# Performance work log

Hardware: AMD Instinct MI355X
Metric: run time of the kernel (lower is better)

The kernel has to match this reference:

```python
import jax, jax.numpy as jnp
from jax import lax
import numpy as np

RF = 1024   # receptive field
MGC = 60    # mgc feature size
UPS = 200   # upsample factor
MIX = 10    # num mixtures
FS = 256    # filter size
F = 2       # mgc frames
N = F * UPS
SQRT_HALF = 0.70710678118


def setup_inputs() -> dict:
    key = jax.random.key(0)
    ks = jax.random.split(key, 30)
    g = lambda i, shape, s=0.05: jax.random.normal(ks[i], shape, dtype=jnp.float32) * s
    return dict(
        signal=g(0, (N + RF,), 0.3),
        mgc=g(1, (F, MGC), 1.0),
        cond_w=g(2, (MGC * UPS, MGC)), cond_b=g(3, (MGC * UPS,)),
        l0_win=g(4, (FS, 1, 2)), l0_bin=g(5, (FS,)),
        l0_wg=g(6, (FS, 1, 2)), l0_bg=g(7, (FS,)),
        l0_wr=g(8, (FS, 1, 2)), l0_br=g(9, (FS,)),
        lw_in=g(10, (9, FS, FS, 2)), lb_in=g(11, (9, FS)),
        lw_g=g(12, (9, FS, FS, 2)), lb_g=g(13, (9, FS)),
        lw_r=g(14, (9, FS, FS, 2)), lb_r=g(15, (9, FS)),
        cw_in=g(16, (10, FS, MGC)), cb_in=g(17, (10, FS)),
        cw_g=g(18, (10, FS, MGC)), cb_g=g(19, (10, FS)),
        pre_w=g(20, (256, FS)), pre_b=g(21, (256,)),
        mean_w=g(22, (MIX, 256)), mean_b=g(23, (MIX,)),
        std_w=g(24, (MIX, 256)), std_b=g(25, (MIX,)),
        logit_w=g(26, (MIX, 256)), logit_b=g(27, (MIX,)),
    )


def _cond_conv(x, cond, win, bin_, wg, bg, wr, br, wci, bci, wcg, bcg):
    # x: [N, Cin, L]; cond: [N, MGC] -> out: [N, FS, L//2]
    conv = lambda w, b: lax.conv_general_dilated(
        x, w, window_strides=(2,), padding='VALID',
        dimension_numbers=('NCH', 'OIH', 'NCH')) + b[None, :, None]
    it = jnp.tanh(conv(win, bin_) + (cond @ wci.T + bci)[:, :, None])
    gt = jax.nn.sigmoid(conv(wg, bg) + (cond @ wcg.T + bcg)[:, :, None])
    return (it * gt + conv(wr, br)) * SQRT_HALF


def _forward(signal, mgc, cond_w, cond_b,
             l0_win, l0_bin, l0_wg, l0_bg, l0_wr, l0_br,
             lw_in, lb_in, lw_g, lb_g, lw_r, lb_r,
             cw_in, cb_in, cw_g, cb_g,
             pre_w, pre_b, mean_w, mean_b, std_w, std_b, logit_w, logit_b):
    n = signal.shape[0] - RF
    # sliding windows: [n, 1, RF]
    idx = jnp.arange(n)[:, None] + jnp.arange(RF)[None, :]
    x = signal[idx][:, None, :]
    # conditioning: [F, MGC] -> [F, MGC*UPS] -> [F*UPS, MGC]
    cond = jnp.tanh(mgc @ cond_w.T + cond_b).reshape(-1, MGC)
    # WaveNet stack: 10 stride-2 gated conv layers, L: 1024 -> 1
    x = _cond_conv(x, cond, l0_win, l0_bin, l0_wg, l0_bg, l0_wr, l0_br,
                   cw_in[0], cb_in[0], cw_g[0], cb_g[0])
    for i in range(9):
        x = _cond_conv(x, cond, lw_in[i], lb_in[i], lw_g[i], lb_g[i],
                       lw_r[i], lb_r[i], cw_in[i + 1], cb_in[i + 1],
                       cw_g[i + 1], cb_g[i + 1])
    pre = jax.nn.relu(x[:, :, 0] @ pre_w.T + pre_b)  # [n, 256]
    mean = pre @ mean_w.T + mean_b
    stdev = pre @ std_w.T + std_b
    logits = pre @ logit_w.T + logit_b
    return mean, stdev, logits


def reference(signal, mgc, cond_w, cond_b,
              l0_win, l0_bin, l0_wg, l0_bg, l0_wr, l0_br,
              lw_in, lb_in, lw_g, lb_g, lw_r, lb_r,
              cw_in, cb_in, cw_g, cb_g,
              pre_w, pre_b, mean_w, mean_b, std_w, std_b, logit_w, logit_b):
    return _forward(signal, mgc, cond_w, cond_b,
                    l0_win, l0_bin, l0_wg, l0_bg, l0_wr, l0_br,
                    lw_in, lb_in, lw_g, lb_g, lw_r, lb_r,
                    cw_in, cb_in, cw_g, cb_g,
                    pre_w, pre_b, mean_w, mean_b, std_w, std_b,
                    logit_w, logit_b)
```

## Files before the change

kernel.cpp:

```cpp
#include <hip/hip_runtime.h>

typedef unsigned short u16;
using bf16x8 = __attribute__((ext_vector_type(8))) short;
using f32x4  = __attribute__((ext_vector_type(4))) float;

#define SQRT_HALF 0.70710678118f

__device__ __forceinline__ u16 f2bf(float f) {
    union { float f; unsigned int i; } x; x.f = f;
    unsigned int i = x.i;
    unsigned int r = (i + 0x7FFFu + ((i >> 16) & 1u)) >> 16;
    return (u16)r;
}
__device__ __forceinline__ float bf2f(u16 u) {
    union { unsigned int i; float f; } x; x.i = ((unsigned int)u) << 16; return x.f;
}
__device__ __forceinline__ float sigm(float x) { return 1.0f / (1.0f + __expf(-x)); }
__device__ __forceinline__ float tanh_f(float x) {
    float cx = fminf(fmaxf(x, -12.f), 12.f);
    float e = __expf(2.f * cx);
    return (e - 1.f) / (e + 1.f);
}

__global__ void cond_kernel(const float* __restrict__ mgc, const float* __restrict__ cond_w,
                            const float* __restrict__ cond_b, float* __restrict__ cond2) {
    int j = blockIdx.x * 256 + threadIdx.x;
    if (j >= 24000) return;
    int f = j / 12000, jj = j % 12000;
    float s = cond_b[jj];
    const float* wrow = cond_w + (size_t)jj * 60;
    const float* mrow = mgc + f * 60;
    for (int c = 0; c < 60; ++c) s += mrow[c] * wrow[c];
    float v = tanh_f(s);
    int n = f * 200 + jj / 60, cc = jj % 60;
    cond2[n * 60 + cc] = v;
}

__global__ void condadd_kernel(const float* __restrict__ cond2,
                               const float* __restrict__ cw_in, const float* __restrict__ cb_in,
                               const float* __restrict__ cw_g,  const float* __restrict__ cb_g,
                               const float* __restrict__ l0_bin, const float* __restrict__ lb_in,
                               const float* __restrict__ l0_bg,  const float* __restrict__ lb_g,
                               float* __restrict__ ca_in, float* __restrict__ ca_g) {
    int idx = blockIdx.x * 256 + threadIdx.x;
    if (idx >= 10 * 400 * 256) return;
    int co = idx & 255;
    int n  = (idx >> 8) % 400;
    int l  = idx / (400 * 256);
    float si = cb_in[l * 256 + co] + (l == 0 ? l0_bin[co] : lb_in[(l - 1) * 256 + co]);
    float sg = cb_g [l * 256 + co] + (l == 0 ? l0_bg [co] : lb_g [(l - 1) * 256 + co]);
    const float* cn = cond2 + n * 60;
    const float* wi = cw_in + (size_t)(l * 256 + co) * 60;
    const float* wg = cw_g  + (size_t)(l * 256 + co) * 60;
    for (int c = 0; c < 60; ++c) {
        float cv = cn[c];
        si += cv * wi[c];
        sg += cv * wg[c];
    }
    ca_in[idx] = si;
    ca_g[idx]  = sg;
}

__global__ void wreorder_kernel(const float* __restrict__ lw_in, const float* __restrict__ lw_g,
                                const float* __restrict__ lw_r, u16* __restrict__ Wg) {
    int idx = blockIdx.x * 256 + threadIdx.x;
    if (idx >= 9 * 256 * 512) return;
    int kk = idx & 511;
    int co = (idx >> 9) & 255;
    int l  = idx >> 17;
    int k = kk >> 8, ci = kk & 255;
    size_t src = ((size_t)(l * 256 + co) * 256 + ci) * 2 + k;
    size_t dst = (size_t)l * 3 * 131072 + (size_t)co * 512 + kk;
    Wg[dst]              = f2bf(lw_in[src]);
    Wg[dst + 131072]     = f2bf(lw_g[src]);
    Wg[dst + 2 * 131072] = f2bf(lw_r[src]);
}

__global__ void l0_kernel(const float* __restrict__ signal,
                          const float* __restrict__ l0_win, const float* __restrict__ l0_wg,
                          const float* __restrict__ l0_wr,  const float* __restrict__ l0_br,
                          const float* __restrict__ ca_in0, const float* __restrict__ ca_g0,
                          u16* __restrict__ Y0, int n_start) {
    int b = blockIdx.x;
    int tg = b & 127, n_local = b >> 7;
    int n = n_start + n_local;
    int ci = threadIdx.x;
    float wi0 = l0_win[ci * 2], wi1 = l0_win[ci * 2 + 1];
    float wg0 = l0_wg [ci * 2], wg1 = l0_wg [ci * 2 + 1];
    float wr0 = l0_wr [ci * 2], wr1 = l0_wr [ci * 2 + 1];
    float cain = ca_in0[n * 256 + ci], cag = ca_g0[n * 256 + ci], br = l0_br[ci];
    for (int i = 0; i < 4; ++i) {
        int t = tg * 4 + i;
        float s0 = signal[n + 2 * t];
        float s1 = signal[n + 2 * t + 1];
        float vin = wi0 * s0 + wi1 * s1 + cain;
        float vg  = wg0 * s0 + wg1 * s1 + cag;
        float vr  = wr0 * s0 + wr1 * s1 + br;
        float o = (tanh_f(vin) * sigm(vg) + vr) * SQRT_HALF;
        Y0[((size_t)n_local * 512 + t) * 256 + ci] = f2bf(o);
    }
}

__global__ __launch_bounds__(256, 2) void gemm_layer_kernel(
        const u16* __restrict__ A, const u16* __restrict__ Wg,
        const float* __restrict__ ca_in, const float* __restrict__ ca_g,
        const float* __restrict__ br, u16* __restrict__ Y,
        int M, int lg, int n_start) {
    __shared__ u16 Alds[2][128 * 64];
    __shared__ u16 Blds[2][192 * 64];
    int m0  = blockIdx.x * 128;
    int co0 = blockIdx.y * 64;
    int tid = threadIdx.x;
    int lane = tid & 63, wave = tid >> 6;
    int wm = wave & 1, wc = wave >> 1;
    int q = lane >> 4, r16 = lane & 15;

    const u16* agp[4]; int alof[4];
    #pragma unroll
    for (int i = 0; i < 4; ++i) {
        int chunk = tid + i * 256;
        int row = chunk >> 3, c8 = chunk & 7;
        int m = m0 + row;
        int msafe = m < M ? m : (M - 1);
        agp[i] = A + (size_t)msafe * 512 + c8 * 8;
        alof[i] = row * 64 + ((c8 ^ (row & 7)) * 8);
    }
    const u16* bgp[6]; int blof[6];
    #pragma unroll
    for (int i = 0; i < 6; ++i) {
        int chunk = tid + i * 256;
        int row = chunk >> 3, c8 = chunk & 7;
        int conv = row >> 6, col = row & 63;
        bgp[i] = Wg + ((size_t)conv * 256 + co0 + col) * 512 + c8 * 8;
        blof[i] = row * 64 + ((c8 ^ (row & 7)) * 8);
    }

    uint4 ra[4], rb[6];
    #pragma unroll
    for (int i = 0; i < 4; ++i) ra[i] = *(const uint4*)(agp[i]);
    #pragma unroll
    for (int i = 0; i < 6; ++i) rb[i] = *(const uint4*)(bgp[i]);
    #pragma unroll
    for (int i = 0; i < 4; ++i) *(uint4*)(&Alds[0][alof[i]]) = ra[i];
    #pragma unroll
    for (int i = 0; i < 6; ++i) *(uint4*)(&Blds[0][blof[i]]) = rb[i];
    asm volatile("s_waitcnt lgkmcnt(0)\n\ts_barrier" ::: "memory");

    f32x4 acc[3][4][2] = {};

    for (int kt = 0; kt < 8; ++kt) {
        int cur = kt & 1;
        if (kt < 7) {
            #pragma unroll
            for (int i = 0; i < 4; ++i) ra[i] = *(const uint4*)(agp[i] + (kt + 1) * 64);
            #pragma unroll
            for (int i = 0; i < 6; ++i) rb[i] = *(const uint4*)(bgp[i] + (kt + 1) * 64);
        }
        #pragma unroll
        for (int ks = 0; ks < 2; ++ks) {
            int kc = ks * 4 + q;
            bf16x8 af[4], bfr[3][2];
            #pragma unroll
            for (int ms = 0; ms < 4; ++ms) {
                int row = wm * 64 + ms * 16 + r16;
                af[ms] = *(const bf16x8*)(&Alds[cur][row * 64 + (kc ^ (row & 7)) * 8]);
            }
            #pragma unroll
            for (int cv = 0; cv < 3; ++cv)
                #pragma unroll
                for (int cs = 0; cs < 2; ++cs) {
                    int row = cv * 64 + wc * 32 + cs * 16 + r16;
                    bfr[cv][cs] = *(const bf16x8*)(&Blds[cur][row * 64 + (kc ^ (row & 7)) * 8]);
                }
            #pragma unroll
            for (int cv = 0; cv < 3; ++cv)
                #pragma unroll
                for (int ms = 0; ms < 4; ++ms)
                    #pragma unroll
                    for (int cs = 0; cs < 2; ++cs)
                        acc[cv][ms][cs] = __builtin_amdgcn_mfma_f32_16x16x32_bf16(
                            af[ms], bfr[cv][cs], acc[cv][ms][cs], 0, 0, 0);
        }
        asm volatile("s_barrier" ::: "memory");
        if (kt < 7) {
            #pragma unroll
            for (int i = 0; i < 4; ++i) *(uint4*)(&Alds[cur ^ 1][alof[i]]) = ra[i];
            #pragma unroll
            for (int i = 0; i < 6; ++i) *(uint4*)(&Blds[cur ^ 1][blof[i]]) = rb[i];
        }
        asm volatile("s_waitcnt lgkmcnt(0)\n\ts_barrier" ::: "memory");
    }

    #pragma unroll
    for (int ms = 0; ms < 4; ++ms) {
        #pragma unroll
        for (int reg = 0; reg < 4; ++reg) {
            int m = m0 + wm * 64 + ms * 16 + q * 4 + reg;
            if (m >= M) continue;
            int n = n_start + (m >> lg);
            #pragma unroll
            for (int cs = 0; cs < 2; ++cs) {
                int co = co0 + wc * 32 + cs * 16 + r16;
                float vin = acc[0][ms][cs][reg] + ca_in[n * 256 + co];
                float vg  = acc[1][ms][cs][reg] + ca_g [n * 256 + co];
                float vr  = acc[2][ms][cs][reg] + br[co];
                float o = (tanh_f(vin) * sigm(vg) + vr) * SQRT_HALF;
                Y[(size_t)m * 256 + co] = f2bf(o);
            }
        }
    }
}

__global__ __launch_bounds__(256) void head_kernel(
        const u16* __restrict__ Y9, const float* __restrict__ pre_w, const float* __restrict__ pre_b,
        const float* __restrict__ mean_w, const float* __restrict__ mean_b,
        const float* __restrict__ std_w,  const float* __restrict__ std_b,
        const float* __restrict__ logit_w, const float* __restrict__ logit_b,
        float* __restrict__ out, int n_start) {
    __shared__ float xin[256];
    __shared__ float pre[256];
    int n_local = blockIdx.x;
    int n = n_start + n_local;
    int t = threadIdx.x;
    xin[t] = bf2f(Y9[(size_t)n_local * 256 + t]);
    __syncthreads();
    float s = pre_b[t];
    const float* wrow = pre_w + (size_t)t * 256;
    for (int c = 0; c < 256; ++c) s += xin[c] * wrow[c];
    pre[t] = fmaxf(s, 0.f);
    __syncthreads();
    if (t < 30) {
        int head = t / 10, mix = t % 10;
        const float* w  = head == 0 ? mean_w : (head == 1 ? std_w : logit_w);
        const float* bb = head == 0 ? mean_b : (head == 1 ? std_b : logit_b);
        float s2 = bb[mix];
        const float* wr = w + mix * 256;
        for (int c = 0; c < 256; ++c) s2 += pre[c] * wr[c];
        out[head * 4000 + n * 10 + mix] = s2;
    }
}

extern "C" void kernel_launch(void* const* d_in, const int* in_sizes, int n_in,
                              void* d_out, int out_size, void* d_ws, size_t ws_size,
                              hipStream_t stream) {
    const float* signal  = (const float*)d_in[0];
    const float* mgc     = (const float*)d_in[1];
    const float* cond_w  = (const float*)d_in[2];
    const float* cond_b  = (const float*)d_in[3];
    const float* l0_win  = (const float*)d_in[4];
    const float* l0_bin  = (const float*)d_in[5];
    const float* l0_wg   = (const float*)d_in[6];
    const float* l0_bg   = (const float*)d_in[7];
    const float* l0_wr   = (const float*)d_in[8];
    const float* l0_br   = (const float*)d_in[9];
    const float* lw_in   = (const float*)d_in[10];
    const float* lb_in   = (const float*)d_in[11];
    const float* lw_g    = (const float*)d_in[12];
    const float* lb_g    = (const float*)d_in[13];
    const float* lw_r    = (const float*)d_in[14];
    const float* lb_r    = (const float*)d_in[15];
    const float* cw_in   = (const float*)d_in[16];
    const float* cb_in   = (const float*)d_in[17];
    const float* cw_g    = (const float*)d_in[18];
    const float* cb_g    = (const float*)d_in[19];
    const float* pre_w   = (const float*)d_in[20];
    const float* pre_b   = (const float*)d_in[21];
    const float* mean_w  = (const float*)d_in[22];
    const float* mean_b  = (const float*)d_in[23];
    const float* std_w   = (const float*)d_in[24];
    const float* std_b   = (const float*)d_in[25];
    const float* logit_w = (const float*)d_in[26];
    const float* logit_b = (const float*)d_in[27];
    float* out = (float*)d_out;

    char* p = (char*)d_ws;
    auto alloc = [&](size_t bytes) -> char* {
        char* r = p; p += (bytes + 255) & ~(size_t)255; return r;
    };
    u16*   Wg    = (u16*)alloc(7077888);
    float* ca_in = (float*)alloc(4096000);
    float* ca_g  = (float*)alloc(4096000);
    float* cond2 = (float*)alloc(96000);
    size_t fixedBytes = (size_t)(p - (char*)d_ws);

    int c = 1;
    while (c < 16 && fixedBytes + (104857600ull + 52428800ull) / c + 4096 > ws_size) c <<= 1;
    u16* bufA = (u16*)alloc(104857600ull / c);
    u16* bufB = (u16*)alloc(52428800ull / c);
    int n_count = 400 / c;

    cond_kernel<<<94, 256, 0, stream>>>(mgc, cond_w, cond_b, cond2);
    condadd_kernel<<<4000, 256, 0, stream>>>(cond2, cw_in, cb_in, cw_g, cb_g,
                                             l0_bin, lb_in, l0_bg, lb_g, ca_in, ca_g);
    wreorder_kernel<<<4608, 256, 0, stream>>>(lw_in, lw_g, lw_r, Wg);

    for (int ch = 0; ch < c; ++ch) {
        int n_start = ch * n_count;
        l0_kernel<<<n_count * 128, 256, 0, stream>>>(signal, l0_win, l0_wg, l0_wr, l0_br,
                                                     ca_in, ca_g, bufA, n_start);
        u16* src = bufA;
        u16* dst = bufB;
        for (int layer = 1; layer <= 9; ++layer) {
            int lg = 9 - layer;
            int M = n_count << lg;
            dim3 grid((M + 127) / 128, 4);
            gemm_layer_kernel<<<grid, 256, 0, stream>>>(
                src, Wg + (size_t)(layer - 1) * 3 * 131072,
                ca_in + (size_t)layer * 102400, ca_g + (size_t)layer * 102400,
                lb_r + (layer - 1) * 256, dst, M, lg, n_start);
            u16* tswap = src; src = dst; dst = tswap;
        }
        head_kernel<<<n_count, 256, 0, stream>>>(src, pre_w, pre_b, mean_w, mean_b,
                                                 std_w, std_b, logit_w, logit_b, out, n_start);
    }
}
```

Before: 596.1 us.

## Use direct global-to-LDS loads with BK=32 pipeline, block swizzle, fast rcp

Rewrites the GEMM layer main loop to load A and B tiles straight into LDS via global_load_lds in 32-wide K chunks with a double-buffered vmcnt-based pipeline. This removes the register staging round-trip, halves LDS footprint per stage so three blocks can share a CU, and raises MFMA priority with setprio. It also remaps block indices so groups of eight M tiles share a co tile for L2 reuse, and replaces divisions in tanh/sigmoid with v_rcp_f32. The cost is more barriers per K step and slightly lower precision in the activations.

```diff
diff --git a/kernel.cpp b/kernel.cpp
--- a/kernel.cpp
+++ b/kernel.cpp
@@ -15,11 +15,23 @@
 __device__ __forceinline__ float bf2f(u16 u) {
     union { unsigned int i; float f; } x; x.i = ((unsigned int)u) << 16; return x.f;
 }
-__device__ __forceinline__ float sigm(float x) { return 1.0f / (1.0f + __expf(-x)); }
+__device__ __forceinline__ float fastrcp(float x) {
+    float r; asm("v_rcp_f32 %0, %1" : "=v"(r) : "v"(x)); return r;
+}
+__device__ __forceinline__ float sigm(float x) {
+    return fastrcp(1.0f + __expf(-x));
+}
 __device__ __forceinline__ float tanh_f(float x) {
     float cx = fminf(fmaxf(x, -12.f), 12.f);
     float e = __expf(2.f * cx);
-    return (e - 1.f) / (e + 1.f);
+    return 1.0f - 2.0f * fastrcp(e + 1.0f);
+}
+
+__device__ __forceinline__ void gld16(const u16* g, u16* l) {
+    __builtin_amdgcn_global_load_lds(
+        (const __attribute__((address_space(1))) void*)g,
+        (__attribute__((address_space(3))) void*)l,
+        16, 0, 0);
 }
 
 __global__ void cond_kernel(const float* __restrict__ mgc, const float* __restrict__ cond_w,
@@ -101,95 +113,106 @@
     }
 }
 
-__global__ __launch_bounds__(256, 2) void gemm_layer_kernel(
+__global__ __launch_bounds__(256, 3) void gemm_layer_kernel(
         const u16* __restrict__ A, const u16* __restrict__ Wg,
         const float* __restrict__ ca_in, const float* __restrict__ ca_g,
         const float* __restrict__ br, u16* __restrict__ Y,
         int M, int lg, int n_start) {
-    __shared__ u16 Alds[2][128 * 64];
-    __shared__ u16 Blds[2][192 * 64];
-    int m0  = blockIdx.x * 128;
-    int co0 = blockIdx.y * 64;
+    __shared__ __attribute__((aligned(16))) u16 A0[128 * 32];
+    __shared__ __attribute__((aligned(16))) u16 A1[128 * 32];
+    __shared__ __attribute__((aligned(16))) u16 B0[192 * 32];
+    __shared__ __attribute__((aligned(16))) u16 B1[192 * 32];
+
+    int mtiles = (M + 127) >> 7;
+    int b = blockIdx.x;
+    int mtile, cotile;
+    if ((mtiles & 7) == 0) {
+        int g = b >> 5, r = b & 31;
+        mtile  = g * 8 + (r & 7);
+        cotile = r >> 3;
+    } else {
+        mtile = b >> 2; cotile = b & 3;
+    }
+    int m0  = mtile * 128;
+    int co0 = cotile * 64;
     int tid = threadIdx.x;
     int lane = tid & 63, wave = tid >> 6;
     int wm = wave & 1, wc = wave >> 1;
     int q = lane >> 4, r16 = lane & 15;
 
-    const u16* agp[4]; int alof[4];
+    const u16* agp[2]; unsigned aoff[2];
     #pragma unroll
-    for (int i = 0; i < 4; ++i) {
-        int chunk = tid + i * 256;
-        int row = chunk >> 3, c8 = chunk & 7;
+    for (int i = 0; i < 2; ++i) {
+        int c = i * 256 + tid;
+        int row = c >> 2, s = c & 3;
         int m = m0 + row;
         int msafe = m < M ? m : (M - 1);
-        agp[i] = A + (size_t)msafe * 512 + c8 * 8;
-        alof[i] = row * 64 + ((c8 ^ (row & 7)) * 8);
-    }
-    const u16* bgp[6]; int blof[6];
+        agp[i] = A + (size_t)msafe * 512 + (s ^ ((row >> 1) & 3)) * 8;
+        aoff[i] = (unsigned)c * 8;
+    }
+    const u16* bgp[3]; unsigned boff[3];
     #pragma unroll
-    for (int i = 0; i < 6; ++i) {
-        int chunk = tid + i * 256;
-        int row = chunk >> 3, c8 = chunk & 7;
+    for (int i = 0; i < 3; ++i) {
+        int c = i * 256 + tid;
+        int row = c >> 2, s = c & 3;
         int conv = row >> 6, col = row & 63;
-        bgp[i] = Wg + ((size_t)conv * 256 + co0 + col) * 512 + c8 * 8;
-        blof[i] = row * 64 + ((c8 ^ (row & 7)) * 8);
-    }
-
-    uint4 ra[4], rb[6];
+        bgp[i] = Wg + ((size_t)conv * 256 + co0 + col) * 512 + (s ^ ((row >> 1) & 3)) * 8;
+        boff[i] = (unsigned)c * 8;
+    }
+
+    f32x4 acc[3][4][2] = {};
+
+    auto doIssue = [&](int ktn, u16* Al, u16* Bl) {
+        #pragma unroll
+        for (int i = 0; i < 2; ++i) gld16(agp[i] + ktn * 32, &Al[aoff[i]]);
+        #pragma unroll
+        for (int i = 0; i < 3; ++i) gld16(bgp[i] + ktn * 32, &Bl[boff[i]]);
+    };
+    auto doComp = [&](const u16* Al, const u16* Bl) {
+        bf16x8 af[4], bfr[3][2];
+        #pragma unroll
+        for (int ms = 0; ms < 4; ++ms) {
+            int row = wm * 64 + ms * 16 + r16;
+            af[ms] = *(const bf16x8*)(&Al[row * 32 + ((q ^ ((row >> 1) & 3)) * 8)]);
+        }
+        #pragma unroll
+        for (int cv = 0; cv < 3; ++cv)
+            #pragma unroll
+            for (int cs = 0; cs < 2; ++cs) {
+                int row = cv * 64 + wc * 32 + cs * 16 + r16;
+                bfr[cv][cs] = *(const bf16x8*)(&Bl[row * 32 + ((q ^ ((row >> 1) & 3)) * 8)]);
+            }
+        __builtin_amdgcn_s_setprio(1);
+        #pragma unroll
+        for (int cv = 0; cv < 3; ++cv)
+            #pragma unroll
+            for (int ms = 0; ms < 4; ++ms)
+                #pragma unroll
+                for (int cs = 0; cs < 2; ++cs)
+                    acc[cv][ms][cs] = __builtin_amdgcn_mfma_f32_16x16x32_bf16(
+                        af[ms], bfr[cv][cs], acc[cv][ms][cs], 0, 0, 0);
+        __builtin_amdgcn_s_setprio(0);
+    };
+
+    doIssue(0, A0, B0);
+    doIssue(1, A1, B1);
+    asm volatile("s_waitcnt vmcnt(5)\n\ts_barrier" ::: "memory");
+
     #pragma unroll
-    for (int i = 0; i < 4; ++i) ra[i] = *(const uint4*)(agp[i]);
-    #pragma unroll
-    for (int i = 0; i < 6; ++i) rb[i] = *(const uint4*)(bgp[i]);
-    #pragma unroll
-    for (int i = 0; i < 4; ++i) *(uint4*)(&Alds[0][alof[i]]) = ra[i];
-    #pragma unroll
-    for (int i = 0; i < 6; ++i) *(uint4*)(&Blds[0][blof[i]]) = rb[i];
+    for (int kt2 = 0; kt2 < 7; ++kt2) {
+        doComp(A0, B0);
+        asm volatile("s_waitcnt lgkmcnt(0)\n\ts_barrier" ::: "memory");
+        doIssue(2 * kt2 + 2, A0, B0);
+        asm volatile("s_waitcnt vmcnt(5)\n\ts_barrier" ::: "memory");
+        doComp(A1, B1);
+        asm volatile("s_waitcnt lgkmcnt(0)\n\ts_barrier" ::: "memory");
+        doIssue(2 * kt2 + 3, A1, B1);
+        asm volatile("s_waitcnt vmcnt(5)\n\ts_barrier" ::: "memory");
+    }
+    doComp(A0, B0);
     asm volatile("s_waitcnt lgkmcnt(0)\n\ts_barrier" ::: "memory");
-
-    f32x4 acc[3][4][2] = {};
-
-    for (int kt = 0; kt < 8; ++kt) {
-        int cur = kt & 1;
-        if (kt < 7) {
-            #pragma unroll
-            for (int i = 0; i < 4; ++i) ra[i] = *(const uint4*)(agp[i] + (kt + 1) * 64);
-            #pragma unroll
-            for (int i = 0; i < 6; ++i) rb[i] = *(const uint4*)(bgp[i] + (kt + 1) * 64);
-        }
-        #pragma unroll
-        for (int ks = 0; ks < 2; ++ks) {
-            int kc = ks * 4 + q;
-            bf16x8 af[4], bfr[3][2];
-            #pragma unroll
-            for (int ms = 0; ms < 4; ++ms) {
-                int row = wm * 64 + ms * 16 + r16;
-                af[ms] = *(const bf16x8*)(&Alds[cur][row * 64 + (kc ^ (row & 7)) * 8]);
-            }
-            #pragma unroll
-            for (int cv = 0; cv < 3; ++cv)
-                #pragma unroll
-                for (int cs = 0; cs < 2; ++cs) {
-                    int row = cv * 64 + wc * 32 + cs * 16 + r16;
-                    bfr[cv][cs] = *(const bf16x8*)(&Blds[cur][row * 64 + (kc ^ (row & 7)) * 8]);
-                }
-            #pragma unroll
-            for (int cv = 0; cv < 3; ++cv)
-                #pragma unroll
-                for (int ms = 0; ms < 4; ++ms)
-                    #pragma unroll
-                    for (int cs = 0; cs < 2; ++cs)
-                        acc[cv][ms][cs] = __builtin_amdgcn_mfma_f32_16x16x32_bf16(
-                            af[ms], bfr[cv][cs], acc[cv][ms][cs], 0, 0, 0);
-        }
-        asm volatile("s_barrier" ::: "memory");
-        if (kt < 7) {
-            #pragma unroll
-            for (int i = 0; i < 4; ++i) *(uint4*)(&Alds[cur ^ 1][alof[i]]) = ra[i];
-            #pragma unroll
-            for (int i = 0; i < 6; ++i) *(uint4*)(&Blds[cur ^ 1][blof[i]]) = rb[i];
-        }
-        asm volatile("s_waitcnt lgkmcnt(0)\n\ts_barrier" ::: "memory");
-    }
+    asm volatile("s_waitcnt vmcnt(0)\n\ts_barrier" ::: "memory");
+    doComp(A1, B1);
 
     #pragma unroll
     for (int ms = 0; ms < 4; ++ms) {
@@ -303,8 +326,8 @@
         for (int layer = 1; layer <= 9; ++layer) {
             int lg = 9 - layer;
             int M = n_count << lg;
-            dim3 grid((M + 127) / 128, 4);
-            gemm_layer_kernel<<<grid, 256, 0, stream>>>(
+            int mtiles = (M + 127) / 128;
+            gemm_layer_kernel<<<mtiles * 4, 256, 0, stream>>>(
                 src, Wg + (size_t)(layer - 1) * 3 * 131072,
                 ca_in + (size_t)layer * 102400, ca_g + (size_t)layer * 102400,
                 lb_r + (layer - 1) * 256, dst, M, lg, n_start);
```

New measurement: 511.9 us. 1.16x faster.
